# Kernel tuning notes

Hardware: AMD Instinct MI355X
Metric: run time of the kernel (lower is better)

The kernel has to match this reference:

```python
import jax, jax.numpy as jnp
import numpy as np


def setup_inputs() -> dict:
    key = jax.random.key(0)
    k1, k2 = jax.random.split(key)
    bs, seq, hidden = 128, 4096, 128
    decoder_state_t = jax.random.normal(k1, (bs, hidden), dtype=jnp.float32)
    encoder_states = jax.random.normal(k2, (bs, seq, hidden), dtype=jnp.float32)
    return {"decoder_state_t": decoder_state_t, "encoder_states": encoder_states}


def reference(decoder_state_t, encoder_states):
    # score[b,s] = sum_h dec[b,h] * enc[b,s,h]  (batched matvec, avoids tile)
    score = jnp.einsum('bh,bsh->bs', decoder_state_t, encoder_states)
    attn_prob = jax.nn.softmax(score, axis=-1)
    # context[b,h] = sum_s attn_prob[b,s] * enc[b,s,h]
    context = jnp.einsum('bs,bsh->bh', attn_prob, encoder_states)
    return (attn_prob, context)
```

## Files before the change

kernel.cpp:

```cpp
#include <hip/hip_runtime.h>
#include <math.h>

#define B_ 128
#define S_ 4096
#define H_ 128
#define SPLITS_ 8
#define CHUNK_ (S_ / SPLITS_)
#define NPART_ (H_ + 2)

__global__ __launch_bounds__(256) void s2s_attn_pass1(
    const float* __restrict__ dec, const float* __restrict__ enc,
    float* __restrict__ score_out, float* __restrict__ part_out) {
  const int blk = blockIdx.x;
  const int b = blk / SPLITS_;
  const int split = blk - b * SPLITS_;
  const int t = threadIdx.x;
  const int w = t >> 6;
  const int lane = t & 63;
  const int half = lane >> 5;
  const int l32 = lane & 31;

  __shared__ float s_score[CHUNK_];
  __shared__ float s_m[4];
  __shared__ float s_l[4];
  __shared__ float s_ctx[4][H_];

  const float4 dv = *reinterpret_cast<const float4*>(dec + b * H_ + l32 * 4);
  const float* encb = enc + (size_t)b * S_ * H_ + (size_t)split * CHUNK_ * H_;

  float m = -INFINITY, l = 0.f;
  float cx = 0.f, cy = 0.f, cz = 0.f, cw = 0.f;

  for (int i = 0; i < CHUNK_ / 8; ++i) {
    const int sl = i * 8 + w * 2;
    const float4 e = *reinterpret_cast<const float4*>(
        encb + (size_t)sl * H_ + lane * 4);
    float p = e.x * dv.x + e.y * dv.y + e.z * dv.z + e.w * dv.w;
    p += __shfl_xor(p, 1);
    p += __shfl_xor(p, 2);
    p += __shfl_xor(p, 4);
    p += __shfl_xor(p, 8);
    p += __shfl_xor(p, 16);
    if (l32 == 0) s_score[sl + half] = p;
    const float mn = fmaxf(m, p);
    const float corr = __expf(m - mn);
    const float wt = __expf(p - mn);
    l = l * corr + wt;
    cx = cx * corr + wt * e.x;
    cy = cy * corr + wt * e.y;
    cz = cz * corr + wt * e.z;
    cw = cw * corr + wt * e.w;
    m = mn;
  }

  const float m_o = __shfl_xor(m, 32);
  const float l_o = __shfl_xor(l, 32);
  const float cx_o = __shfl_xor(cx, 32);
  const float cy_o = __shfl_xor(cy, 32);
  const float cz_o = __shfl_xor(cz, 32);
  const float cw_o = __shfl_xor(cw, 32);
  const float M = fmaxf(m, m_o);
  const float ea = __expf(m - M);
  const float eb = __expf(m_o - M);
  if (lane == 0) { s_m[w] = M; s_l[w] = l * ea + l_o * eb; }
  if (half == 0) {
    s_ctx[w][l32 * 4 + 0] = cx * ea + cx_o * eb;
    s_ctx[w][l32 * 4 + 1] = cy * ea + cy_o * eb;
    s_ctx[w][l32 * 4 + 2] = cz * ea + cz_o * eb;
    s_ctx[w][l32 * 4 + 3] = cw * ea + cw_o * eb;
  }
  __syncthreads();

  float* part = part_out + (size_t)blk * NPART_;
  if (t < H_) {
    const float m0 = s_m[0], m1 = s_m[1], m2 = s_m[2], m3 = s_m[3];
    const float Mb = fmaxf(fmaxf(m0, m1), fmaxf(m2, m3));
    const float e0 = __expf(m0 - Mb), e1 = __expf(m1 - Mb);
    const float e2 = __expf(m2 - Mb), e3 = __expf(m3 - Mb);
    if (t == 0) {
      part[0] = Mb;
      part[1] = s_l[0] * e0 + s_l[1] * e1 + s_l[2] * e2 + s_l[3] * e3;
    }
    part[2 + t] = s_ctx[0][t] * e0 + s_ctx[1][t] * e1 +
                  s_ctx[2][t] * e2 + s_ctx[3][t] * e3;
  }

  float* so = score_out + (size_t)b * S_ + (size_t)split * CHUNK_;
  for (int j = t; j < CHUNK_; j += 256) so[j] = s_score[j];
}

__global__ __launch_bounds__(256) void s2s_attn_pass2(
    float* __restrict__ attn, float* __restrict__ ctx_out,
    const float* __restrict__ part_in) {
  const int b = blockIdx.x;
  const int t = threadIdx.x;
  const float* base = part_in + (size_t)b * SPLITS_ * NPART_;

  float mv[SPLITS_], lv[SPLITS_], ex[SPLITS_];
  float M = -INFINITY;
  for (int p = 0; p < SPLITS_; ++p) {
    mv[p] = base[p * NPART_];
    lv[p] = base[p * NPART_ + 1];
    M = fmaxf(M, mv[p]);
  }
  float L = 0.f;
  for (int p = 0; p < SPLITS_; ++p) {
    ex[p] = __expf(mv[p] - M);
    L += lv[p] * ex[p];
  }
  const float invL = 1.0f / L;

  if (t < H_) {
    float c = 0.f;
    for (int p = 0; p < SPLITS_; ++p) c += base[p * NPART_ + 2 + t] * ex[p];
    ctx_out[(size_t)b * H_ + t] = c * invL;
  }

  float* ab = attn + (size_t)b * S_;
  for (int j = t; j < S_; j += 256) ab[j] = __expf(ab[j] - M) * invL;
}

extern "C" void kernel_launch(void* const* d_in, const int* in_sizes, int n_in,
                              void* d_out, int out_size, void* d_ws, size_t ws_size,
                              hipStream_t stream) {
  const float* dec = (const float*)d_in[0];
  const float* enc = (const float*)d_in[1];
  float* out = (float*)d_out;
  float* attn = out;
  float* ctx = out + (size_t)B_ * S_;
  float* part = (float*)d_ws;

  s2s_attn_pass1<<<dim3(B_ * SPLITS_), dim3(256), 0, stream>>>(dec, enc, attn, part);
  s2s_attn_pass2<<<dim3(B_), dim3(256), 0, stream>>>(attn, ctx, part);
}
```

Measured before the change: 366.6 us.

## Batch four encoder rows per iteration and double the sequence splits

Each iteration of the pass-1 loop now issues four independent float4 loads, one for each of four rows. It also does one online-softmax rescale per group of four scores instead of one per score. The loop is fully unrolled. The sequence is split into 16 chunks instead of 8, so twice as many blocks are launched. The goal is more memory-level parallelism and occupancy for this bandwidth-bound kernel, at the cost of more registers per thread and a larger partial buffer for pass 2 to combine.

```diff
diff --git a/kernel.cpp b/kernel.cpp
--- a/kernel.cpp
+++ b/kernel.cpp
@@ -4,7 +4,7 @@
 #define B_ 128
 #define S_ 4096
 #define H_ 128
-#define SPLITS_ 8
+#define SPLITS_ 16
 #define CHUNK_ (S_ / SPLITS_)
 #define NPART_ (H_ + 2)
 
@@ -31,25 +31,47 @@
   float m = -INFINITY, l = 0.f;
   float cx = 0.f, cy = 0.f, cz = 0.f, cw = 0.f;
 
-  for (int i = 0; i < CHUNK_ / 8; ++i) {
-    const int sl = i * 8 + w * 2;
-    const float4 e = *reinterpret_cast<const float4*>(
-        encb + (size_t)sl * H_ + lane * 4);
-    float p = e.x * dv.x + e.y * dv.y + e.z * dv.z + e.w * dv.w;
-    p += __shfl_xor(p, 1);
-    p += __shfl_xor(p, 2);
-    p += __shfl_xor(p, 4);
-    p += __shfl_xor(p, 8);
-    p += __shfl_xor(p, 16);
-    if (l32 == 0) s_score[sl + half] = p;
-    const float mn = fmaxf(m, p);
+#pragma unroll
+  for (int i = 0; i < CHUNK_ / 32; ++i) {
+    const int base = i * 32 + w * 8;
+    const float4 e0 = *reinterpret_cast<const float4*>(
+        encb + (size_t)(base + 0 + half) * H_ + l32 * 4);
+    const float4 e1 = *reinterpret_cast<const float4*>(
+        encb + (size_t)(base + 2 + half) * H_ + l32 * 4);
+    const float4 e2 = *reinterpret_cast<const float4*>(
+        encb + (size_t)(base + 4 + half) * H_ + l32 * 4);
+    const float4 e3 = *reinterpret_cast<const float4*>(
+        encb + (size_t)(base + 6 + half) * H_ + l32 * 4);
+
+    float p0 = e0.x * dv.x + e0.y * dv.y + e0.z * dv.z + e0.w * dv.w;
+    float p1 = e1.x * dv.x + e1.y * dv.y + e1.z * dv.z + e1.w * dv.w;
+    float p2 = e2.x * dv.x + e2.y * dv.y + e2.z * dv.z + e2.w * dv.w;
+    float p3 = e3.x * dv.x + e3.y * dv.y + e3.z * dv.z + e3.w * dv.w;
+#pragma unroll
+    for (int s = 1; s <= 16; s <<= 1) {
+      p0 += __shfl_xor(p0, s);
+      p1 += __shfl_xor(p1, s);
+      p2 += __shfl_xor(p2, s);
+      p3 += __shfl_xor(p3, s);
+    }
+    if (l32 == 0) {
+      s_score[base + 0 + half] = p0;
+      s_score[base + 2 + half] = p1;
+      s_score[base + 4 + half] = p2;
+      s_score[base + 6 + half] = p3;
+    }
+    const float mb = fmaxf(fmaxf(p0, p1), fmaxf(p2, p3));
+    const float mn = fmaxf(m, mb);
     const float corr = __expf(m - mn);
-    const float wt = __expf(p - mn);
-    l = l * corr + wt;
-    cx = cx * corr + wt * e.x;
-    cy = cy * corr + wt * e.y;
-    cz = cz * corr + wt * e.z;
-    cw = cw * corr + wt * e.w;
+    const float w0 = __expf(p0 - mn);
+    const float w1 = __expf(p1 - mn);
+    const float w2 = __expf(p2 - mn);
+    const float w3 = __expf(p3 - mn);
+    l = l * corr + (w0 + w1 + w2 + w3);
+    cx = cx * corr + w0 * e0.x + w1 * e1.x + w2 * e2.x + w3 * e3.x;
+    cy = cy * corr + w0 * e0.y + w1 * e1.y + w2 * e2.y + w3 * e3.y;
+    cz = cz * corr + w0 * e0.z + w1 * e1.z + w2 * e2.z + w3 * e3.z;
+    cw = cw * corr + w0 * e0.w + w1 * e1.w + w2 * e2.w + w3 * e3.w;
     m = mn;
   }
 
@@ -86,7 +108,7 @@
   }
 
   float* so = score_out + (size_t)b * S_ + (size_t)split * CHUNK_;
-  for (int j = t; j < CHUNK_; j += 256) so[j] = s_score[j];
+  if (t < CHUNK_) so[t] = s_score[t];
 }
 
 __global__ __launch_bounds__(256) void s2s_attn_pass2(
@@ -98,12 +120,14 @@
 
   float mv[SPLITS_], lv[SPLITS_], ex[SPLITS_];
   float M = -INFINITY;
+#pragma unroll
   for (int p = 0; p < SPLITS_; ++p) {
     mv[p] = base[p * NPART_];
     lv[p] = base[p * NPART_ + 1];
     M = fmaxf(M, mv[p]);
   }
   float L = 0.f;
+#pragma unroll
   for (int p = 0; p < SPLITS_; ++p) {
     ex[p] = __expf(mv[p] - M);
     L += lv[p] * ex[p];
@@ -112,11 +136,13 @@
 
   if (t < H_) {
     float c = 0.f;
+#pragma unroll
     for (int p = 0; p < SPLITS_; ++p) c += base[p * NPART_ + 2 + t] * ex[p];
     ctx_out[(size_t)b * H_ + t] = c * invL;
   }
 
   float* ab = attn + (size_t)b * S_;
+#pragma unroll 4
   for (int j = t; j < S_; j += 256) ab[j] = __expf(ab[j] - M) * invL;
 }
 
```

After: 360.6 us (median of 2 runs). No clear change (-1.6%).
